# Kernel tuning notes

Measured on AMD Instinct MI355X. Metric: run time of the kernel, lower is better.

The kernel has to match this reference:

```python
import jax, jax.numpy as jnp
import numpy as np

B, N, OBS_DIM = 64, 512, 128
HIDDEN_DIM, MESSAGE_DIM, ACTION_DIM = 256, 128, 16


def _dense_params(key, din, dout):
    kw, kb = jax.random.split(key)
    W = jax.random.normal(kw, (din, dout), jnp.float32) * 0.02
    b = jnp.zeros((dout,), jnp.float32)
    return W, b


def setup_inputs() -> dict:
    key = jax.random.key(0)
    ks = jax.random.split(key, 12)
    obs_batch = jax.random.normal(ks[0], (B, N, OBS_DIM), jnp.float32)
    dones_batch = jnp.zeros((B, N), jnp.bool_)
    We, be = _dense_params(ks[1], OBS_DIM, HIDDEN_DIM)
    Wc, bc = _dense_params(ks[2], HIDDEN_DIM, MESSAGE_DIM // 4)
    Wn, bn = _dense_params(ks[3], HIDDEN_DIM, MESSAGE_DIM // 2)
    Wb, bb = _dense_params(ks[4], HIDDEN_DIM, MESSAGE_DIM // 4)
    Wi, bi = _dense_params(ks[5], HIDDEN_DIM, 1)
    Wq, bq = _dense_params(ks[6], HIDDEN_DIM, MESSAGE_DIM)
    Wk, bk = _dense_params(ks[7], MESSAGE_DIM, MESSAGE_DIM)
    Wv, bv = _dense_params(ks[8], MESSAGE_DIM, MESSAGE_DIM)
    Wp, bp = _dense_params(ks[9], HIDDEN_DIM + MESSAGE_DIM, HIDDEN_DIM)
    Wa, ba = _dense_params(ks[10], HIDDEN_DIM, ACTION_DIM)
    Wcr, bcr = _dense_params(ks[11], HIDDEN_DIM, 1)
    return {"obs_batch": obs_batch, "dones_batch": dones_batch,
            "We": We, "be": be, "Wc": Wc, "bc": bc, "Wn": Wn, "bn": bn,
            "Wb": Wb, "bb": bb, "Wi": Wi, "bi": bi, "Wq": Wq, "bq": bq,
            "Wk": Wk, "bk": bk, "Wv": Wv, "bv": bv, "Wp": Wp, "bp": bp,
            "Wa": Wa, "ba": ba, "Wcr": Wcr, "bcr": bcr}


def reference(obs_batch, dones_batch, We, be, Wc, bc, Wn, bn, Wb, bb, Wi, bi,
              Wq, bq, Wk, bk, Wv, bv, Wp, bp, Wa, ba, Wcr, bcr):
    dense = lambda x, W, b: x @ W + b
    encoded = jax.nn.relu(dense(obs_batch, We, be))                 # [B,N,H]
    messages = jnp.concatenate([dense(encoded, Wc, bc),
                                dense(encoded, Wn, bn),
                                dense(encoded, Wb, bb)], axis=-1)   # [B,N,M]
    importance = jax.nn.sigmoid(dense(encoded, Wi, bi))             # [B,N,1]
    Q = dense(encoded, Wq, bq)
    K = dense(messages, Wk, bk)
    V = dense(messages, Wv, bv)
    scores = jnp.einsum('bqd,bkd->bqk', Q, K) / jnp.sqrt(jnp.float32(MESSAGE_DIM))
    importance_weights = importance * jnp.transpose(importance, (0, 2, 1))  # [B,N,N]
    scores = scores * importance_weights
    norms = jnp.linalg.norm(obs_batch, axis=-1, keepdims=True)      # [B,N,1]
    obs_sim = jnp.einsum('bid,bjd->bij', obs_batch, obs_batch)
    obs_sim = obs_sim / (norms + 1e-08)
    obs_sim = obs_sim / (jnp.transpose(norms, (0, 2, 1)) + 1e-08)
    scores = scores + obs_sim * 0.5
    attn = jax.nn.softmax(scores, axis=-1)
    aggregated = jnp.einsum('bqk,bkd->bqd', attn, V)                # [B,N,M]
    combined = jnp.concatenate([encoded, aggregated], axis=-1)
    x = jax.nn.relu(dense(combined, Wp, bp))
    logits = dense(x, Wa, ba)
    value = dense(x, Wcr, bcr).squeeze(-1)
    return (logits, value)
```

## Files before the change

### kernel.cpp

```cpp
#include <hip/hip_runtime.h>
#include <math.h>


typedef __attribute__((ext_vector_type(8))) short short8;
typedef __attribute__((ext_vector_type(4))) float f32x4;

#define RSQRT_D 0.08838834764831843f
#define MFMA __builtin_amdgcn_mfma_f32_16x16x32_bf16

__device__ __forceinline__ unsigned short f2bf(float f) {
  union { float f; unsigned u; } v; v.f = f;
  return (unsigned short)((v.u + 0x7FFFu + ((v.u >> 16) & 1u)) >> 16);
}
__device__ __forceinline__ unsigned pack2(float a, float b) {
  return (unsigned)f2bf(a) | ((unsigned)f2bf(b) << 16);
}
__device__ __forceinline__ short8 ld8(const unsigned short* p) {
  return *(const short8*)p;
}
__device__ __forceinline__ void gl16(const unsigned short* g,
                                     unsigned short* l) {
  __builtin_amdgcn_global_load_lds(
      (const __attribute__((address_space(1))) unsigned int*)(const void*)g,
      (__attribute__((address_space(3))) unsigned int*)(void*)l, 16, 0, 0);
}

__global__ __launch_bounds__(256) void prep_all(
    const float* __restrict__ obs, const float* __restrict__ We,
    const float* __restrict__ Wq, const float* __restrict__ Wk,
    const float* __restrict__ Wv, const float* __restrict__ Wp,
    const float* __restrict__ Wc, const float* __restrict__ Wn,
    const float* __restrict__ Wb, const float* __restrict__ bc,
    const float* __restrict__ bn, const float* __restrict__ bb,
    const float* __restrict__ Wa, const float* __restrict__ Wcr,
    const float* __restrict__ ba, const float* __restrict__ bcr,
    unsigned short* __restrict__ WeT, unsigned short* __restrict__ Wmq,
    unsigned short* __restrict__ Wkv, unsigned short* __restrict__ WpT,
    unsigned short* __restrict__ WaCrT, float* __restrict__ bm,
    unsigned short* __restrict__ obs_bf, unsigned short* __restrict__ As,
    unsigned short* __restrict__ Bs, float* __restrict__ logits,
    float* __restrict__ value, float* __restrict__ imp_raw) {
  const int bid = blockIdx.x, tid = threadIdx.x;
  if (bid < 929) {
    int idx = bid * 256 + tid;
    if (idx < 32768) {
      int n = idx >> 7, k = idx & 127;
      WeT[idx] = f2bf(We[k * 256 + n]);
    } else if (idx < 65536) {
      int i = idx - 32768;
      int d = i >> 8, h = i & 255;
      float v = (d < 32)   ? Wc[h * 32 + d]
              : (d < 96)   ? Wn[h * 64 + (d - 32)]
                           : Wb[h * 32 + (d - 96)];
      Wmq[i] = f2bf(v);
    } else if (idx < 98304) {
      int i = idx - 65536;
      int n = i >> 8, k = i & 255;
      Wmq[32768 + i] = f2bf(Wq[k * 128 + n]);
    } else if (idx < 114688) {
      int i = idx - 98304;
      int n = i >> 7, k = i & 127;
      Wkv[i] = f2bf(Wk[k * 128 + n]);
    } else if (idx < 131072) {
      int i = idx - 114688;
      int n = i >> 7, k = i & 127;
      Wkv[16384 + i] = f2bf(Wv[k * 128 + n]);
    } else if (idx < 229376) {
      int i = idx - 131072;
      int n = i / 384, k = i - n * 384;
      WpT[i] = f2bf(Wp[k * 256 + n]);
    } else if (idx < 237568) {
      int i = idx - 229376;
      int n = i >> 8, k = i & 255;
      float v = (n < 16) ? Wa[k * 16 + n] : (n == 16) ? Wcr[k] : 0.f;
      WaCrT[i] = f2bf(v);
    } else if (idx < 237696) {
      int i = idx - 237568;
      bm[i] = (i < 32) ? bc[i] : (i < 96) ? bn[i - 32] : bb[i - 96];
    }
  } else if (bid < 9121) {
    int t = (bid - 929) * 4 + (tid >> 6);
    int lane = tid & 63;
    const float* row = obs + (size_t)t * 128;
    float2 o = *(const float2*)(row + lane * 2);
    float s2 = o.x * o.x + o.y * o.y;
#pragma unroll
    for (int off = 1; off < 64; off <<= 1) s2 += __shfl_xor(s2, off);
    float inv = 1.f / (sqrtf(s2) + 1e-8f);
    ((unsigned*)obs_bf)[(size_t)t * 64 + lane] = pack2(o.x, o.y);
    ((unsigned*)As)[(size_t)t * 128 + 64 + lane] =
        pack2(o.x * 0.5f * inv, o.y * 0.5f * inv);
    ((unsigned*)Bs)[(size_t)t * 128 + 64 + lane] = pack2(o.x * inv, o.y * inv);
  } else if (bid < 11297) {
    int i = (bid - 9121) * 256 + tid;
    if (i < 524288) logits[i] = ba[i & 15];
    else value[i - 524288] = bcr[0];
  } else {
    imp_raw[(bid - 11297) * 256 + tid] = 0.f;
  }
}

template <int MODE, int IMP>
__device__ __forceinline__ void emit(unsigned short* out, int ldc,
                                     const float* bias, const float* sg,
                                     int rowb, int col, const f32x4& a,
                                     float* ip, const float* Wi, int gcol) {
  const float bv = bias[col];
  if constexpr (MODE == 3) {
    uint2 o;
    o.x = pack2(a[0] + bv, a[1] + bv);
    o.y = pack2(a[2] + bv, a[3] + bv);
    *(uint2*)(out + ((size_t)(rowb >> 9) * 128 + col) * 512 + (rowb & 511)) = o;
  } else {
    float wv = 0.f;
    if constexpr (IMP) wv = Wi[gcol];
#pragma unroll
    for (int r = 0; r < 4; ++r) {
      float v = a[r] + bv;
      if constexpr (MODE == 1) v = fmaxf(v, 0.f);
      if constexpr (MODE == 2) v *= sg[r];
      out[(size_t)(rowb + r) * ldc + col] = f2bf(v);
      if constexpr (IMP) ip[r] += v * wv;
    }
  }
}

template <int M0, int M1, int IMP>
__global__ __launch_bounds__(256, 2) void gemm_t(
    const unsigned short* __restrict__ A1, int lda1, int K1,
    const unsigned short* __restrict__ A2, int lda2, int Ktot,
    const unsigned short* __restrict__ Bt, int ldb,
    const float* __restrict__ bias0, const float* __restrict__ bias1,
    const float* __restrict__ raw, const float* __restrict__ bi, float mult,
    const float* __restrict__ Wi, float* __restrict__ imp_out,
    unsigned short* __restrict__ out0, int ldc0,
    unsigned short* __restrict__ out1, int ldc1, int xsplit) {
  __shared__ unsigned short Asr[8192];
  __shared__ unsigned short Bsr[8192];
  const int tid = threadIdx.x, lane = tid & 63, wave = tid >> 6;
  const int quad = lane >> 4, l16 = lane & 15;
  const int wm = wave & 1, wn = wave >> 1;
  const int bm = blockIdx.y * 128, bn = blockIdx.x * 128;
  const int srow = tid >> 3, slc = tid & 7;

  f32x4 acc[4][4];
#pragma unroll
  for (int i = 0; i < 4; ++i)
#pragma unroll
    for (int j = 0; j < 4; ++j) acc[i][j] = (f32x4){0.f, 0.f, 0.f, 0.f};

  for (int kt = 0; kt < Ktot; kt += 64) {
    const unsigned short* Ap;
    int lda, kloc;
    if (kt < K1) { Ap = A1; lda = lda1; kloc = kt; }
    else         { Ap = A2; lda = lda2; kloc = kt - K1; }
#pragma unroll
    for (int i = 0; i < 4; ++i) {
      int row = i * 32 + srow;
      gl16(Ap + (size_t)(bm + row) * lda + kloc + ((slc ^ (row & 7)) << 3),
           Asr + i * 2048 + wave * 512);
      gl16(Bt + (size_t)(bn + row) * ldb + kt + ((slc ^ (row & 7)) << 3),
           Bsr + i * 2048 + wave * 512);
    }
    __syncthreads();
#pragma unroll
    for (int ks = 0; ks < 2; ++ks) {
      short8 af[4], bf[4];
#pragma unroll
      for (int mi = 0; mi < 4; ++mi) {
        int row = wm * 64 + mi * 16 + l16;
        af[mi] = *(const short8*)&Asr[row * 64 + (((ks * 4 + quad) ^ (row & 7)) << 3)];
      }
#pragma unroll
      for (int ni = 0; ni < 4; ++ni) {
        int row = wn * 64 + ni * 16 + l16;
        bf[ni] = *(const short8*)&Bsr[row * 64 + (((ks * 4 + quad) ^ (row & 7)) << 3)];
      }
#pragma unroll
      for (int mi = 0; mi < 4; ++mi)
#pragma unroll
        for (int ni = 0; ni < 4; ++ni)
          acc[mi][ni] = MFMA(af[mi], bf[ni], acc[mi][ni], 0, 0, 0);
    }
    __syncthreads();
  }

  float bi0 = 0.f;
  if constexpr (M0 == 2 || M1 == 2) bi0 = bi[0];
#pragma unroll
  for (int mi = 0; mi < 4; ++mi) {
    const int rowb = bm + wm * 64 + mi * 16 + quad * 4;
    float sg[4] = {0.f, 0.f, 0.f, 0.f};
    if constexpr (M0 == 2 || M1 == 2) {
#pragma unroll
      for (int r = 0; r < 4; ++r)
        sg[r] = mult / (1.f + __expf(-(raw[rowb + r] + bi0)));
    }
    float ip[4] = {0.f, 0.f, 0.f, 0.f};
#pragma unroll
    for (int ni = 0; ni < 4; ++ni) {
      const int col = bn + wn * 64 + ni * 16 + l16;
      if (col < xsplit)
        emit<M0, IMP>(out0, ldc0, bias0, sg, rowb, col, acc[mi][ni], ip, Wi, col);
      else
        emit<M1, 0>(out1, ldc1, bias1, sg, rowb, col - xsplit, acc[mi][ni],
                    nullptr, nullptr, 0);
    }
    if constexpr (IMP) {
#pragma unroll
      for (int r = 0; r < 4; ++r) {
#pragma unroll
        for (int off = 1; off < 16; off <<= 1)
          ip[r] += __shfl_xor(ip[r], off);
      }
      if (l16 == 0) {
#pragma unroll
        for (int r = 0; r < 4; ++r) atomicAdd(&imp_out[rowb + r], ip[r]);
      }
    }
  }
}

__global__ __launch_bounds__(256, 3) void flash4(
    const unsigned short* __restrict__ As, const unsigned short* __restrict__ Bs,
    const unsigned short* __restrict__ vT, unsigned short* __restrict__ agg) {
  __shared__ unsigned short Ub[16384];
  __shared__ unsigned short Pp[4096];
  __shared__ float redm[2][32];
  __shared__ float reds[2][32];
  const int tid = threadIdx.x, lane = tid & 63, wave = tid >> 6;
  const int quad = lane >> 4, l16 = lane & 15;
  const int wm = wave & 1, wn = wave >> 1;
  const int b = blockIdx.x & 63;
  const int qt = blockIdx.x >> 6;
  const size_t tok0 = (size_t)b * 512 + qt * 32;
  const int srow = tid >> 4, slc = tid & 15;

  short8 af[8];
#pragma unroll
  for (int kc = 0; kc < 8; ++kc)
    af[kc] = ld8(As + (tok0 + wm * 16 + l16) * 256 + kc * 32 + quad * 8);

  f32x4 s[4][4];
#pragma unroll
  for (int kt = 0; kt < 4; ++kt)
#pragma unroll
    for (int nt = 0; nt < 4; ++nt) s[kt][nt] = (f32x4){0.f, 0.f, 0.f, 0.f};

#pragma unroll
  for (int kt = 0; kt < 4; ++kt) {
#pragma unroll
    for (int kh = 0; kh < 2; ++kh) {
      __syncthreads();
#pragma unroll
      for (int i = 0; i < 8; ++i) {
        int row = i * 16 + srow;
        gl16(Bs + ((size_t)b * 512 + kt * 128 + row) * 256 + kh * 128 +
                 ((slc ^ (row & 15)) << 3),
             Ub + i * 2048 + wave * 512);
      }
      __syncthreads();
#pragma unroll
      for (int kk = 0; kk < 4; ++kk) {
        short8 bfr[4];
#pragma unroll
        for (int nt = 0; nt < 4; ++nt) {
          int rr = wn * 64 + nt * 16 + l16;
          bfr[nt] = *(const short8*)&Ub[rr * 128 + (((kk * 4 + quad) ^ (rr & 15)) << 3)];
        }
#pragma unroll
        for (int nt = 0; nt < 4; ++nt)
          s[kt][nt] = MFMA(af[kh * 4 + kk], bfr[nt], s[kt][nt], 0, 0, 0);
      }
    }
  }

  const int rbase = wm * 16 + quad * 4;
  float mt[4];
#pragma unroll
  for (int r = 0; r < 4; ++r) {
    float mv = -1e30f;
#pragma unroll
    for (int kt = 0; kt < 4; ++kt)
#pragma unroll
      for (int nt = 0; nt < 4; ++nt) mv = fmaxf(mv, s[kt][nt][r]);
#pragma unroll
    for (int off = 1; off < 16; off <<= 1) mv = fmaxf(mv, __shfl_xor(mv, off));
    mt[r] = mv;
  }
  if (l16 == 0) {
#pragma unroll
    for (int r = 0; r < 4; ++r) redm[wn][rbase + r] = mt[r];
  }
  __syncthreads();
  float lsum[4];
#pragma unroll
  for (int r = 0; r < 4; ++r) {
    float mfull = fmaxf(mt[r], redm[1 ^ wn][rbase + r]);
    float sum = 0.f;
#pragma unroll
    for (int kt = 0; kt < 4; ++kt)
#pragma unroll
      for (int nt = 0; nt < 4; ++nt) {
        float p = __expf(s[kt][nt][r] - mfull);
        s[kt][nt][r] = p;
        sum += p;
      }
#pragma unroll
    for (int off = 1; off < 16; off <<= 1) sum += __shfl_xor(sum, off);
    lsum[r] = sum;
  }
  if (l16 == 0) {
#pragma unroll
    for (int r = 0; r < 4; ++r) reds[wn][rbase + r] = lsum[r];
  }
  __syncthreads();
  float linv[4];
#pragma unroll
  for (int r = 0; r < 4; ++r)
    linv[r] = 1.0f / (lsum[r] + reds[1 ^ wn][rbase + r]);

  f32x4 oacc[4];
#pragma unroll
  for (int nt = 0; nt < 4; ++nt) oacc[nt] = (f32x4){0.f, 0.f, 0.f, 0.f};
#pragma unroll
  for (int vt = 0; vt < 4; ++vt) {
    __syncthreads();
#pragma unroll
    for (int nt = 0; nt < 4; ++nt) {
      const int col = wn * 64 + nt * 16 + l16;
#pragma unroll
      for (int r = 0; r < 4; ++r) {
        const int row = rbase + r;
        Pp[row * 128 + (((col >> 3) ^ (row & 15)) << 3) + (col & 7)] =
            f2bf(s[vt][nt][r]);
      }
    }
#pragma unroll
    for (int i = 0; i < 8; ++i) {
      int row = i * 16 + srow;
      gl16(vT + ((size_t)b * 128 + row) * 512 + vt * 128 +
               ((slc ^ (row & 15)) << 3),
           Ub + i * 2048 + wave * 512);
    }
    __syncthreads();
#pragma unroll
    for (int kk = 0; kk < 4; ++kk) {
      const int prow = wm * 16 + l16;
      short8 pa = *(const short8*)&Pp[prow * 128 + (((kk * 4 + quad) ^ (prow & 15)) << 3)];
#pragma unroll
      for (int nt = 0; nt < 4; ++nt) {
        int rr = wn * 64 + nt * 16 + l16;
        short8 vb = *(const short8*)&Ub[rr * 128 + (((kk * 4 + quad) ^ (rr & 15)) << 3)];
        oacc[nt] = MFMA(pa, vb, oacc[nt], 0, 0, 0);
      }
    }
  }
#pragma unroll
  for (int nt = 0; nt < 4; ++nt) {
    const int col = wn * 64 + nt * 16 + l16;
#pragma unroll
    for (int r = 0; r < 4; ++r)
      agg[(tok0 + rbase + r) * 128 + col] = f2bf(oacc[nt][r] * linv[r]);
  }
}

__global__ __launch_bounds__(256, 2) void xh_gemm(
    const unsigned short* __restrict__ enc, const unsigned short* __restrict__ agg,
    const unsigned short* __restrict__ WpT, const float* __restrict__ bp,
    const unsigned short* __restrict__ WaCrT, float* __restrict__ logits,
    float* __restrict__ value) {
  __shared__ unsigned short sm[16384];
  unsigned short* Asr = sm;
  unsigned short* Bsr = sm + 8192;
  const int tid = threadIdx.x, lane = tid & 63, wave = tid >> 6;
  const int quad = lane >> 4, l16 = lane & 15;
  const int wm = wave & 1, wn = wave >> 1;
  const int bm = blockIdx.y * 128, bn = blockIdx.x * 128;
  const int srow = tid >> 3, slc = tid & 7;

  f32x4 acc[4][4];
#pragma unroll
  for (int i = 0; i < 4; ++i)
#pragma unroll
    for (int j = 0; j < 4; ++j) acc[i][j] = (f32x4){0.f, 0.f, 0.f, 0.f};

  for (int kt = 0; kt < 384; kt += 64) {
    const unsigned short* Ap;
    int lda, kloc;
    if (kt < 256) { Ap = enc; lda = 256; kloc = kt; }
    else          { Ap = agg; lda = 128; kloc = kt - 256; }
#pragma unroll
    for (int i = 0; i < 4; ++i) {
      int row = i * 32 + srow;
      gl16(Ap + (size_t)(bm + row) * lda + kloc + ((slc ^ (row & 7)) << 3),
           Asr + i * 2048 + wave * 512);
      gl16(WpT + (size_t)(bn + row) * 384 + kt + ((slc ^ (row & 7)) << 3),
           Bsr + i * 2048 + wave * 512);
    }
    __syncthreads();
#pragma unroll
    for (int ks = 0; ks < 2; ++ks) {
      short8 af[4], bf[4];
#pragma unroll
      for (int mi = 0; mi < 4; ++mi) {
        int row = wm * 64 + mi * 16 + l16;
        af[mi] = *(const short8*)&Asr[row * 64 + (((ks * 4 + quad) ^ (row & 7)) << 3)];
      }
#pragma unroll
      for (int ni = 0; ni < 4; ++ni) {
        int row = wn * 64 + ni * 16 + l16;
        bf[ni] = *(const short8*)&Bsr[row * 64 + (((ks * 4 + quad) ^ (row & 7)) << 3)];
      }
#pragma unroll
      for (int mi = 0; mi < 4; ++mi)
#pragma unroll
        for (int ni = 0; ni < 4; ++ni)
          acc[mi][ni] = MFMA(af[mi], bf[ni], acc[mi][ni], 0, 0, 0);
    }
    __syncthreads();
  }

#pragma unroll
  for (int mi = 0; mi < 4; ++mi) {
    const int row = wm * 64 + mi * 16 + quad * 4;
#pragma unroll
    for (int ni = 0; ni < 4; ++ni) {
      const int colc = wn * 64 + ni * 16 + l16;
      const float bv = bp[bn + colc];
#pragma unroll
      for (int r = 0; r < 4; ++r) {
        float v = fmaxf(acc[mi][ni][r] + bv, 0.f);
        sm[(row + r) * 128 + (((colc >> 3) ^ ((row + r) & 15)) << 3) + (colc & 7)] =
            f2bf(v);
      }
    }
  }
  __syncthreads();

  f32x4 h[2][2];
#pragma unroll
  for (int i = 0; i < 2; ++i)
#pragma unroll
    for (int j = 0; j < 2; ++j) h[i][j] = (f32x4){0.f, 0.f, 0.f, 0.f};
#pragma unroll
  for (int kc = 0; kc < 4; ++kc) {
    short8 xa[2], wb[2];
#pragma unroll
    for (int hm = 0; hm < 2; ++hm) {
      int row = wave * 32 + hm * 16 + l16;
      xa[hm] = *(const short8*)&sm[row * 128 + (((kc * 4 + quad) ^ (row & 15)) << 3)];
    }
#pragma unroll
    for (int hn = 0; hn < 2; ++hn)
      wb[hn] = ld8(WaCrT + (size_t)(hn * 16 + l16) * 256 + bn + kc * 32 + quad * 8);
#pragma unroll
    for (int hm = 0; hm < 2; ++hm)
#pragma unroll
      for (int hn = 0; hn < 2; ++hn)
        h[hm][hn] = MFMA(xa[hm], wb[hn], h[hm][hn], 0, 0, 0);
  }
#pragma unroll
  for (int hm = 0; hm < 2; ++hm) {
#pragma unroll
    for (int hn = 0; hn < 2; ++hn) {
      const int n = hn * 16 + l16;
#pragma unroll
      for (int r = 0; r < 4; ++r) {
        const int grow = bm + wave * 32 + hm * 16 + quad * 4 + r;
        if (n < 16)
          atomicAdd(&logits[(size_t)grow * 16 + n], h[hm][hn][r]);
        else if (n == 16)
          atomicAdd(&value[grow], h[hm][hn][r]);
      }
    }
  }
}

extern "C" void kernel_launch(void* const* d_in, const int* in_sizes, int n_in,
                              void* d_out, int out_size, void* d_ws,
                              size_t ws_size, hipStream_t stream) {
  const float* obs = (const float*)d_in[0];
  const float* We = (const float*)d_in[2];
  const float* be = (const float*)d_in[3];
  const float* Wc = (const float*)d_in[4];
  const float* bc = (const float*)d_in[5];
  const float* Wn = (const float*)d_in[6];
  const float* bn = (const float*)d_in[7];
  const float* Wb = (const float*)d_in[8];
  const float* bb = (const float*)d_in[9];
  const float* Wi = (const float*)d_in[10];
  const float* bi = (const float*)d_in[11];
  const float* Wq = (const float*)d_in[12];
  const float* bq = (const float*)d_in[13];
  const float* Wk = (const float*)d_in[14];
  const float* bk = (const float*)d_in[15];
  const float* Wv = (const float*)d_in[16];
  const float* bv = (const float*)d_in[17];
  const float* Wp = (const float*)d_in[18];
  const float* bp = (const float*)d_in[19];
  const float* Wa = (const float*)d_in[20];
  const float* ba = (const float*)d_in[21];
  const float* Wcr = (const float*)d_in[22];
  const float* bcr = (const float*)d_in[23];

  char* base = (char*)d_ws;
  unsigned short* enc_bf = (unsigned short*)(base);
  unsigned short* As     = (unsigned short*)(base + 16777216);
  unsigned short* Bs     = (unsigned short*)(base + 33554432);
  unsigned short* obsagg = (unsigned short*)(base + 50331648);
  unsigned short* msg_bf = (unsigned short*)(base + 58720256);
  unsigned short* vT     = (unsigned short*)(base + 75497472);
  float* imp_raw         = (float*)(base + 83886080);
  unsigned short* WeT    = (unsigned short*)(base + 84148224);
  unsigned short* Wmq    = (unsigned short*)(base + 84213760);
  unsigned short* Wkv    = (unsigned short*)(base + 84344832);
  unsigned short* WpT    = (unsigned short*)(base + 84410368);
  float* bmb             = (float*)(base + 84606976);
  unsigned short* WaCrT  = (unsigned short*)(base + 84607488);

  float* logits = (float*)d_out;
  float* value = (float*)d_out + 524288;

  prep_all<<<11425, 256, 0, stream>>>(obs, We, Wq, Wk, Wv, Wp, Wc, Wn, Wb, bc,
                                      bn, bb, Wa, Wcr, ba, bcr, WeT, Wmq, Wkv,
                                      WpT, WaCrT, bmb, obsagg, As, Bs, logits,
                                      value, imp_raw);

  gemm_t<1, 1, 1><<<dim3(2, 256), 256, 0, stream>>>(
      obsagg, 128, 128, nullptr, 0, 128, WeT, 128, be, be, nullptr, nullptr,
      0.f, Wi, imp_raw, enc_bf, 256, enc_bf, 256, 256);
  gemm_t<0, 2, 0><<<dim3(2, 256), 256, 0, stream>>>(
      enc_bf, 256, 256, nullptr, 0, 256, Wmq, 256, bmb, bq, imp_raw, bi,
      RSQRT_D, nullptr, nullptr, msg_bf, 128, As, 256, 128);
  gemm_t<2, 3, 0><<<dim3(2, 256), 256, 0, stream>>>(
      msg_bf, 128, 128, nullptr, 0, 128, Wkv, 128, bk, bv, imp_raw, bi, 1.0f,
      nullptr, nullptr, Bs, 256, vT, 0, 128);

  flash4<<<1024, 256, 0, stream>>>(As, Bs, vT, obsagg);

  xh_gemm<<<dim3(2, 256), 256, 0, stream>>>(enc_bf, obsagg, WpT, bp, WaCrT,
                                            logits, value);
}
```

Before: 199.7 us.

## Fold message projection into K/V weights and merge QKV into one GEMM

```diff
diff --git a/kernel.cpp b/kernel.cpp
--- a/kernel.cpp
+++ b/kernel.cpp
@@ -11,6 +11,10 @@
 __device__ __forceinline__ unsigned short f2bf(float f) {
   union { float f; unsigned u; } v; v.f = f;
   return (unsigned short)((v.u + 0x7FFFu + ((v.u >> 16) & 1u)) >> 16);
+}
+__device__ __forceinline__ float bf2f(unsigned short h) {
+  union { unsigned u; float f; } v; v.u = ((unsigned)h) << 16;
+  return v.f;
 }
 __device__ __forceinline__ unsigned pack2(float a, float b) {
   return (unsigned)f2bf(a) | ((unsigned)f2bf(b) << 16);
@@ -34,12 +38,14 @@
     const float* __restrict__ bn, const float* __restrict__ bb,
     const float* __restrict__ Wa, const float* __restrict__ Wcr,
     const float* __restrict__ ba, const float* __restrict__ bcr,
-    unsigned short* __restrict__ WeT, unsigned short* __restrict__ Wmq,
-    unsigned short* __restrict__ Wkv, unsigned short* __restrict__ WpT,
+    const float* __restrict__ bq, unsigned short* __restrict__ WeT,
+    unsigned short* __restrict__ Wqkv, unsigned short* __restrict__ Wkv,
+    unsigned short* __restrict__ Wm_nt, unsigned short* __restrict__ WpT,
     unsigned short* __restrict__ WaCrT, float* __restrict__ bm,
-    unsigned short* __restrict__ obs_bf, unsigned short* __restrict__ As,
-    unsigned short* __restrict__ Bs, float* __restrict__ logits,
-    float* __restrict__ value, float* __restrict__ imp_raw) {
+    float* __restrict__ bqkv, unsigned short* __restrict__ obs_bf,
+    unsigned short* __restrict__ As, unsigned short* __restrict__ Bs,
+    float* __restrict__ logits, float* __restrict__ value,
+    float* __restrict__ imp_raw) {
   const int bid = blockIdx.x, tid = threadIdx.x;
   if (bid < 929) {
     int idx = bid * 256 + tid;
@@ -48,23 +54,19 @@
       WeT[idx] = f2bf(We[k * 256 + n]);
     } else if (idx < 65536) {
       int i = idx - 32768;
-      int d = i >> 8, h = i & 255;
-      float v = (d < 32)   ? Wc[h * 32 + d]
-              : (d < 96)   ? Wn[h * 64 + (d - 32)]
-                           : Wb[h * 32 + (d - 96)];
-      Wmq[i] = f2bf(v);
+      int n = i >> 8, k = i & 255;
+      Wqkv[i] = f2bf(Wq[k * 128 + n]);
     } else if (idx < 98304) {
       int i = idx - 65536;
-      int n = i >> 8, k = i & 255;
-      Wmq[32768 + i] = f2bf(Wq[k * 128 + n]);
-    } else if (idx < 114688) {
+      int n = i >> 7, k = i & 127;
+      Wkv[i] = f2bf(n < 128 ? Wk[k * 128 + n] : Wv[k * 128 + (n - 128)]);
+    } else if (idx < 131072) {
       int i = idx - 98304;
-      int n = i >> 7, k = i & 127;
-      Wkv[i] = f2bf(Wk[k * 128 + n]);
-    } else if (idx < 131072) {
-      int i = idx - 114688;
-      int n = i >> 7, k = i & 127;
-      Wkv[16384 + i] = f2bf(Wv[k * 128 + n]);
+      int h = i >> 7, m = i & 127;
+      float v = (m < 32)   ? Wc[h * 32 + m]
+              : (m < 96)   ? Wn[h * 64 + (m - 32)]
+                           : Wb[h * 32 + (m - 96)];
+      Wm_nt[i] = f2bf(v);
     } else if (idx < 229376) {
       int i = idx - 131072;
       int n = i / 384, k = i - n * 384;
@@ -77,70 +79,175 @@
     } else if (idx < 237696) {
       int i = idx - 237568;
       bm[i] = (i < 32) ? bc[i] : (i < 96) ? bn[i - 32] : bb[i - 96];
-    }
-  } else if (bid < 9121) {
-    int t = (bid - 929) * 4 + (tid >> 6);
-    int lane = tid & 63;
-    const float* row = obs + (size_t)t * 128;
-    float2 o = *(const float2*)(row + lane * 2);
-    float s2 = o.x * o.x + o.y * o.y;
-#pragma unroll
-    for (int off = 1; off < 64; off <<= 1) s2 += __shfl_xor(s2, off);
-    float inv = 1.f / (sqrtf(s2) + 1e-8f);
-    ((unsigned*)obs_bf)[(size_t)t * 64 + lane] = pack2(o.x, o.y);
-    ((unsigned*)As)[(size_t)t * 128 + 64 + lane] =
-        pack2(o.x * 0.5f * inv, o.y * 0.5f * inv);
-    ((unsigned*)Bs)[(size_t)t * 128 + 64 + lane] = pack2(o.x * inv, o.y * inv);
-  } else if (bid < 11297) {
-    int i = (bid - 9121) * 256 + tid;
+    } else if (idx < 237824) {
+      int i = idx - 237696;
+      bqkv[i] = bq[i];
+    }
+  } else if (bid < 2977) {
+    const int wave = tid >> 6, lane = tid & 63;
+    const int t0 = (bid - 929) * 16 + wave * 4;
+#pragma unroll
+    for (int it = 0; it < 4; ++it) {
+      int t = t0 + it;
+      const float* row = obs + (size_t)t * 128;
+      float2 o = *(const float2*)(row + lane * 2);
+      float s2 = o.x * o.x + o.y * o.y;
+#pragma unroll
+      for (int off = 1; off < 64; off <<= 1) s2 += __shfl_xor(s2, off);
+      float inv = 1.f / (sqrtf(s2) + 1e-8f);
+      ((unsigned*)obs_bf)[(size_t)t * 64 + lane] = pack2(o.x, o.y);
+      ((unsigned*)As)[(size_t)t * 128 + 64 + lane] =
+          pack2(o.x * 0.5f * inv, o.y * 0.5f * inv);
+      ((unsigned*)Bs)[(size_t)t * 128 + 64 + lane] =
+          pack2(o.x * inv, o.y * inv);
+    }
+  } else if (bid < 5153) {
+    int i = (bid - 2977) * 256 + tid;
     if (i < 524288) logits[i] = ba[i & 15];
     else value[i - 524288] = bcr[0];
   } else {
-    imp_raw[(bid - 11297) * 256 + tid] = 0.f;
-  }
-}
-
-template <int MODE, int IMP>
-__device__ __forceinline__ void emit(unsigned short* out, int ldc,
-                                     const float* bias, const float* sg,
-                                     int rowb, int col, const f32x4& a,
-                                     float* ip, const float* Wi, int gcol) {
-  const float bv = bias[col];
-  if constexpr (MODE == 3) {
-    uint2 o;
-    o.x = pack2(a[0] + bv, a[1] + bv);
-    o.y = pack2(a[2] + bv, a[3] + bv);
-    *(uint2*)(out + ((size_t)(rowb >> 9) * 128 + col) * 512 + (rowb & 511)) = o;
+    imp_raw[(bid - 5153) * 256 + tid] = 0.f;
+  }
+}
+
+__global__ __launch_bounds__(256) void prep_wprod(
+    const unsigned short* __restrict__ Wkv,
+    const unsigned short* __restrict__ Wm_nt, const float* __restrict__ bm,
+    const float* __restrict__ bk, const float* __restrict__ bv,
+    unsigned short* __restrict__ Wqkv, float* __restrict__ bqkv) {
+  const int bid = blockIdx.x, tid = threadIdx.x;
+  if (bid < 8) {
+    const int lane = tid & 63, wave = tid >> 6;
+    const int quad = lane >> 4, l16 = lane & 15;
+    const int r0 = bid * 32;
+    f32x4 acc[2][4];
+#pragma unroll
+    for (int i = 0; i < 2; ++i)
+#pragma unroll
+      for (int j = 0; j < 4; ++j) acc[i][j] = (f32x4){0.f, 0.f, 0.f, 0.f};
+#pragma unroll
+    for (int kc = 0; kc < 4; ++kc) {
+      short8 af[2], bf[4];
+#pragma unroll
+      for (int i = 0; i < 2; ++i)
+        af[i] = ld8(Wkv + (size_t)(r0 + i * 16 + l16) * 128 + kc * 32 + quad * 8);
+#pragma unroll
+      for (int j = 0; j < 4; ++j)
+        bf[j] = ld8(Wm_nt + (size_t)(wave * 64 + j * 16 + l16) * 128 + kc * 32 +
+                    quad * 8);
+#pragma unroll
+      for (int i = 0; i < 2; ++i)
+#pragma unroll
+        for (int j = 0; j < 4; ++j)
+          acc[i][j] = MFMA(af[i], bf[j], acc[i][j], 0, 0, 0);
+    }
+#pragma unroll
+    for (int i = 0; i < 2; ++i) {
+      const int row = r0 + i * 16 + quad * 4;
+#pragma unroll
+      for (int j = 0; j < 4; ++j) {
+        const int col = wave * 64 + j * 16 + l16;
+#pragma unroll
+        for (int r = 0; r < 4; ++r)
+          Wqkv[(size_t)(128 + row + r) * 256 + col] = f2bf(acc[i][j][r]);
+      }
+    }
   } else {
-    float wv = 0.f;
-    if constexpr (IMP) wv = Wi[gcol];
+    int i = tid;
+    float acc = (i < 128) ? bk[i] : bv[i - 128];
+    for (int m = 0; m < 128; ++m)
+      acc += bm[m] * bf2f(Wkv[(size_t)i * 128 + m]);
+    bqkv[128 + i] = acc;
+  }
+}
+
+__global__ __launch_bounds__(256, 2) void enc_gemm(
+    const unsigned short* __restrict__ obs_bf,
+    const unsigned short* __restrict__ WeT, const float* __restrict__ be,
+    const float* __restrict__ Wi, unsigned short* __restrict__ enc,
+    float* __restrict__ imp_raw) {
+  __shared__ unsigned short Asr[16384];
+  __shared__ unsigned short Bsr[16384];
+  const int tid = threadIdx.x, lane = tid & 63, wave = tid >> 6;
+  const int quad = lane >> 4, l16 = lane & 15;
+  const int wm = wave & 1, wn = wave >> 1;
+  const int bm0 = blockIdx.y * 128, bn0 = blockIdx.x * 128;
+
+#pragma unroll
+  for (int it = 0; it < 8; ++it) {
+    int c = it * 256 + tid;
+    int row = c >> 4, ch = c & 15;
+    gl16(obs_bf + (size_t)(bm0 + row) * 128 + ((ch ^ (row & 15)) << 3),
+         Asr + it * 2048 + wave * 512);
+    gl16(WeT + (size_t)(bn0 + row) * 128 + ((ch ^ (row & 15)) << 3),
+         Bsr + it * 2048 + wave * 512);
+  }
+  __syncthreads();
+
+  f32x4 acc[4][4];
+#pragma unroll
+  for (int i = 0; i < 4; ++i)
+#pragma unroll
+    for (int j = 0; j < 4; ++j) acc[i][j] = (f32x4){0.f, 0.f, 0.f, 0.f};
+#pragma unroll
+  for (int ks = 0; ks < 4; ++ks) {
+    short8 af[4], bf[4];
+#pragma unroll
+    for (int mi = 0; mi < 4; ++mi) {
+      int row = wm * 64 + mi * 16 + l16;
+      af[mi] = *(const short8*)&Asr[row * 128 + (((ks * 4 + quad) ^ (row & 15)) << 3)];
+    }
+#pragma unroll
+    for (int ni = 0; ni < 4; ++ni) {
+      int row = wn * 64 + ni * 16 + l16;
+      bf[ni] = *(const short8*)&Bsr[row * 128 + (((ks * 4 + quad) ^ (row & 15)) << 3)];
+    }
+#pragma unroll
+    for (int mi = 0; mi < 4; ++mi)
+#pragma unroll
+      for (int ni = 0; ni < 4; ++ni)
+        acc[mi][ni] = MFMA(af[mi], bf[ni], acc[mi][ni], 0, 0, 0);
+  }
+
+#pragma unroll
+  for (int mi = 0; mi < 4; ++mi) {
+    const int rowb = bm0 + wm * 64 + mi * 16 + quad * 4;
+    float ip[4] = {0.f, 0.f, 0.f, 0.f};
+#pragma unroll
+    for (int ni = 0; ni < 4; ++ni) {
+      const int col = bn0 + wn * 64 + ni * 16 + l16;
+      const float bv = be[col], wv = Wi[col];
+#pragma unroll
+      for (int r = 0; r < 4; ++r) {
+        float v = fmaxf(acc[mi][ni][r] + bv, 0.f);
+        enc[(size_t)(rowb + r) * 256 + col] = f2bf(v);
+        ip[r] += v * wv;
+      }
+    }
 #pragma unroll
     for (int r = 0; r < 4; ++r) {
-      float v = a[r] + bv;
-      if constexpr (MODE == 1) v = fmaxf(v, 0.f);
-      if constexpr (MODE == 2) v *= sg[r];
-      out[(size_t)(rowb + r) * ldc + col] = f2bf(v);
-      if constexpr (IMP) ip[r] += v * wv;
-    }
-  }
-}
-
-template <int M0, int M1, int IMP>
-__global__ __launch_bounds__(256, 2) void gemm_t(
-    const unsigned short* __restrict__ A1, int lda1, int K1,
-    const unsigned short* __restrict__ A2, int lda2, int Ktot,
-    const unsigned short* __restrict__ Bt, int ldb,
-    const float* __restrict__ bias0, const float* __restrict__ bias1,
-    const float* __restrict__ raw, const float* __restrict__ bi, float mult,
-    const float* __restrict__ Wi, float* __restrict__ imp_out,
-    unsigned short* __restrict__ out0, int ldc0,
-    unsigned short* __restrict__ out1, int ldc1, int xsplit) {
+#pragma unroll
+      for (int off = 1; off < 16; off <<= 1) ip[r] += __shfl_xor(ip[r], off);
+    }
+    if (l16 == 0) {
+#pragma unroll
+      for (int r = 0; r < 4; ++r) atomicAdd(&imp_raw[rowb + r], ip[r]);
+    }
+  }
+}
+
+__global__ __launch_bounds__(256, 2) void qkv_gemm(
+    const unsigned short* __restrict__ enc, const unsigned short* __restrict__ Wqkv,
+    const float* __restrict__ bqkv, const float* __restrict__ imp_raw,
+    const float* __restrict__ bi, unsigned short* __restrict__ As,
+    unsigned short* __restrict__ Bs, unsigned short* __restrict__ vT) {
   __shared__ unsigned short Asr[8192];
   __shared__ unsigned short Bsr[8192];
   const int tid = threadIdx.x, lane = tid & 63, wave = tid >> 6;
   const int quad = lane >> 4, l16 = lane & 15;
   const int wm = wave & 1, wn = wave >> 1;
-  const int bm = blockIdx.y * 128, bn = blockIdx.x * 128;
+  const int bx = blockIdx.x;
+  const int bm0 = blockIdx.y * 128, bn0 = bx * 128;
   const int srow = tid >> 3, slc = tid & 7;
 
   f32x4 acc[4][4];
@@ -149,17 +256,13 @@
 #pragma unroll
     for (int j = 0; j < 4; ++j) acc[i][j] = (f32x4){0.f, 0.f, 0.f, 0.f};
 
-  for (int kt = 0; kt < Ktot; kt += 64) {
-    const unsigned short* Ap;
-    int lda, kloc;
-    if (kt < K1) { Ap = A1; lda = lda1; kloc = kt; }
-    else         { Ap = A2; lda = lda2; kloc = kt - K1; }
+  for (int kt = 0; kt < 256; kt += 64) {
 #pragma unroll
     for (int i = 0; i < 4; ++i) {
       int row = i * 32 + srow;
-      gl16(Ap + (size_t)(bm + row) * lda + kloc + ((slc ^ (row & 7)) << 3),
+      gl16(enc + (size_t)(bm0 + row) * 256 + kt + ((slc ^ (row & 7)) << 3),
            Asr + i * 2048 + wave * 512);
-      gl16(Bt + (size_t)(bn + row) * ldb + kt + ((slc ^ (row & 7)) << 3),
+      gl16(Wqkv + (size_t)(bn0 + row) * 256 + kt + ((slc ^ (row & 7)) << 3),
            Bsr + i * 2048 + wave * 512);
     }
     __syncthreads();
@@ -185,37 +288,34 @@
     __syncthreads();
   }
 
-  float bi0 = 0.f;
-  if constexpr (M0 == 2 || M1 == 2) bi0 = bi[0];
+  const float bi0 = bi[0];
 #pragma unroll
   for (int mi = 0; mi < 4; ++mi) {
-    const int rowb = bm + wm * 64 + mi * 16 + quad * 4;
-    float sg[4] = {0.f, 0.f, 0.f, 0.f};
-    if constexpr (M0 == 2 || M1 == 2) {
+    const int rowb = bm0 + wm * 64 + mi * 16 + quad * 4;
+    float sg[4];
+    if (bx < 2) {
+      const float mult = (bx == 0) ? RSQRT_D : 1.0f;
 #pragma unroll
       for (int r = 0; r < 4; ++r)
-        sg[r] = mult / (1.f + __expf(-(raw[rowb + r] + bi0)));
-    }
-    float ip[4] = {0.f, 0.f, 0.f, 0.f};
+        sg[r] = mult / (1.f + __expf(-(imp_raw[rowb + r] + bi0)));
+    }
 #pragma unroll
     for (int ni = 0; ni < 4; ++ni) {
-      const int col = bn + wn * 64 + ni * 16 + l16;
-      if (col < xsplit)
-        emit<M0, IMP>(out0, ldc0, bias0, sg, rowb, col, acc[mi][ni], ip, Wi, col);
-      else
-        emit<M1, 0>(out1, ldc1, bias1, sg, rowb, col - xsplit, acc[mi][ni],
-                    nullptr, nullptr, 0);
-    }
-    if constexpr (IMP) {
-#pragma unroll
-      for (int r = 0; r < 4; ++r) {
-#pragma unroll
-        for (int off = 1; off < 16; off <<= 1)
-          ip[r] += __shfl_xor(ip[r], off);
-      }
-      if (l16 == 0) {
-#pragma unroll
-        for (int r = 0; r < 4; ++r) atomicAdd(&imp_out[rowb + r], ip[r]);
+      const int col = wn * 64 + ni * 16 + l16;
+      const float bv = bqkv[bx * 128 + col];
+      if (bx == 0) {
+#pragma unroll
+        for (int r = 0; r < 4; ++r)
+          As[(size_t)(rowb + r) * 256 + col] = f2bf((acc[mi][ni][r] + bv) * sg[r]);
+      } else if (bx == 1) {
+#pragma unroll
+        for (int r = 0; r < 4; ++r)
+          Bs[(size_t)(rowb + r) * 256 + col] = f2bf((acc[mi][ni][r] + bv) * sg[r]);
+      } else {
+        uint2 o;
+        o.x = pack2(acc[mi][ni][0] + bv, acc[mi][ni][1] + bv);
+        o.y = pack2(acc[mi][ni][2] + bv, acc[mi][ni][3] + bv);
+        *(uint2*)(vT + ((size_t)(rowb >> 9) * 128 + col) * 512 + (rowb & 511)) = o;
       }
     }
   }
@@ -509,36 +609,31 @@
   unsigned short* As     = (unsigned short*)(base + 16777216);
   unsigned short* Bs     = (unsigned short*)(base + 33554432);
   unsigned short* obsagg = (unsigned short*)(base + 50331648);
-  unsigned short* msg_bf = (unsigned short*)(base + 58720256);
-  unsigned short* vT     = (unsigned short*)(base + 75497472);
-  float* imp_raw         = (float*)(base + 83886080);
-  unsigned short* WeT    = (unsigned short*)(base + 84148224);
-  unsigned short* Wmq    = (unsigned short*)(base + 84213760);
-  unsigned short* Wkv    = (unsigned short*)(base + 84344832);
-  unsigned short* WpT    = (unsigned short*)(base + 84410368);
-  float* bmb             = (float*)(base + 84606976);
-  unsigned short* WaCrT  = (unsigned short*)(base + 84607488);
+  unsigned short* vT     = (unsigned short*)(base + 58720256);
+  float* imp_raw         = (float*)(base + 67108864);
+  unsigned short* WeT    = (unsigned short*)(base + 67239936);
+  unsigned short* Wqkv   = (unsigned short*)(base + 67305472);
+  unsigned short* Wkv    = (unsigned short*)(base + 67502080);
+  unsigned short* Wm_nt  = (unsigned short*)(base + 67567616);
+  unsigned short* WpT    = (unsigned short*)(base + 67633152);
+  unsigned short* WaCrT  = (unsigned short*)(base + 67829760);
+  float* bmb             = (float*)(base + 67846144);
+  float* bqkv            = (float*)(base + 67846656);
 
   float* logits = (float*)d_out;
   float* value = (float*)d_out + 524288;
 
-  prep_all<<<11425, 256, 0, stream>>>(obs, We, Wq, Wk, Wv, Wp, Wc, Wn, Wb, bc,
-                                      bn, bb, Wa, Wcr, ba, bcr, WeT, Wmq, Wkv,
-                                      WpT, WaCrT, bmb, obsagg, As, Bs, logits,
-                                      value, imp_raw);
-
-  gemm_t<1, 1, 1><<<dim3(2, 256), 256, 0, stream>>>(
-      obsagg, 128, 128, nullptr, 0, 128, WeT, 128, be, be, nullptr, nullptr,
-      0.f, Wi, imp_raw, enc_bf, 256, enc_bf, 256, 256);
-  gemm_t<0, 2, 0><<<dim3(2, 256), 256, 0, stream>>>(
-      enc_bf, 256, 256, nullptr, 0, 256, Wmq, 256, bmb, bq, imp_raw, bi,
-      RSQRT_D, nullptr, nullptr, msg_bf, 128, As, 256, 128);
-  gemm_t<2, 3, 0><<<dim3(2, 256), 256, 0, stream>>>(
-      msg_bf, 128, 128, nullptr, 0, 128, Wkv, 128, bk, bv, imp_raw, bi, 1.0f,
-      nullptr, nullptr, Bs, 256, vT, 0, 128);
-
+  prep_all<<<5281, 256, 0, stream>>>(obs, We, Wq, Wk, Wv, Wp, Wc, Wn, Wb, bc,
+                                     bn, bb, Wa, Wcr, ba, bcr, bq, WeT, Wqkv,
+                                     Wkv, Wm_nt, WpT, WaCrT, bmb, bqkv, obsagg,
+                                     As, Bs, logits, value, imp_raw);
+  prep_wprod<<<9, 256, 0, stream>>>(Wkv, Wm_nt, bmb, bk, bv, Wqkv, bqkv);
+
+  enc_gemm<<<dim3(2, 256), 256, 0, stream>>>(obsagg, WeT, be, Wi, enc_bf,
+                                             imp_raw);
+  qkv_gemm<<<dim3(3, 256), 256, 0, stream>>>(enc_bf, Wqkv, bqkv, imp_raw, bi,
+                                             As, Bs, vT);
   flash4<<<1024, 256, 0, stream>>>(As, Bs, vT, obsagg);
-
   xh_gemm<<<dim3(2, 256), 256, 0, stream>>>(enc_bf, obsagg, WpT, bp, WaCrT,
                                             logits, value);
 }
```

New measurement: 189.1 us. 1.06x faster.
